# Kernel optimization log

Hardware: AMD Instinct MI355X
Metric: run time of the kernel (lower is better)

Reference implementation:

```python
import jax, jax.numpy as jnp
import numpy as np
import math

K = 8       # wavelet order (k)
C = 8       # channels (c)
ALPHA = 64  # retained Fourier modes
L = 0       # coarsest level
B = 32
N = 8192    # power of two


def setup_inputs() -> dict:
    key = jax.random.key(0)
    ks = jax.random.split(key, 14)
    ck = C * K
    scale = 1.0 / (ck * ck)  # matches torch: 1/(c*k)**2
    f32 = jnp.float32
    inp = {
        "x": jax.random.normal(ks[0], (B, N, C, K), dtype=f32),
        # SparseKernelFT1d weights (complex, stored as re/im): scale * rand
        "wA_re": scale * jax.random.uniform(ks[1], (ck, ck, ALPHA), dtype=f32),
        "wA_im": scale * jax.random.uniform(ks[2], (ck, ck, ALPHA), dtype=f32),
        "wB_re": scale * jax.random.uniform(ks[3], (ck, ck, ALPHA), dtype=f32),
        "wB_im": scale * jax.random.uniform(ks[4], (ck, ck, ALPHA), dtype=f32),
        "wC_re": scale * jax.random.uniform(ks[5], (ck, ck, ALPHA), dtype=f32),
        "wC_im": scale * jax.random.uniform(ks[6], (ck, ck, ALPHA), dtype=f32),
        # T0 linear layer (k -> k)
        "T0_w": jax.random.normal(ks[7], (K, K), dtype=f32) / math.sqrt(K),
        "T0_b": 0.01 * jax.random.normal(ks[8], (K,), dtype=f32),
        # Legendre wavelet filter buffers: ec_* are [H0.T;H1.T] / [G0.T;G1.T] (2k,k),
        # rc_* are [H0;G0] / [H1;G1] (2k,k). Stand-ins: random orthonormal-ish matrices
        # scaled like wavelet filters (same math regardless of exact values).
        "ec_s": jax.random.normal(ks[9], (2 * K, K), dtype=f32) / math.sqrt(2 * K),
        "ec_d": jax.random.normal(ks[10], (2 * K, K), dtype=f32) / math.sqrt(2 * K),
        "rc_e": jax.random.normal(ks[11], (2 * K, K), dtype=f32) / math.sqrt(2 * K),
        "rc_o": jax.random.normal(ks[12], (2 * K, K), dtype=f32) / math.sqrt(2 * K),
    }
    return inp


def _sparse_ft(x, w_re, w_im):
    # x: [B, N, c, k] -> spectral mixing over first ALPHA rfft modes
    Bb, Nn, c, k = x.shape
    xv = x.reshape(Bb, Nn, c * k).transpose(0, 2, 1)   # [B, ck, N]
    xf = jnp.fft.rfft(xv)                               # [B, ck, N//2+1] complex
    l = min(ALPHA, Nn // 2 + 1)
    W = (w_re[:, :, :l] + 1j * w_im[:, :, :l]).astype(jnp.complex64)
    of = jnp.einsum('bix,iox->box', xf[:, :, :l], W)
    out_ft = jnp.zeros((Bb, c * k, Nn // 2 + 1), dtype=jnp.complex64).at[:, :, :l].set(of)
    xo = jnp.fft.irfft(out_ft, n=Nn)                    # [B, ck, N] real
    return xo.transpose(0, 2, 1).reshape(Bb, Nn, c, k)


def reference(x, wA_re, wA_im, wB_re, wB_im, wC_re, wC_im, T0_w, T0_b,
              ec_s, ec_d, rc_e, rc_o):
    Bb, Nn, c, k = x.shape
    ns = int(math.floor(math.log2(Nn)))
    Ud, Us = [], []
    # --- decomposition ---
    for _ in range(ns - L):
        xa = jnp.concatenate([x[:, ::2], x[:, 1::2]], axis=-1)  # [B, N/2, c, 2k]
        d = xa @ ec_d                                           # [B, N/2, c, k]
        s = xa @ ec_s
        Ud.append(_sparse_ft(d, wA_re, wA_im) + _sparse_ft(s, wB_re, wB_im))
        Us.append(_sparse_ft(d, wC_re, wC_im))
        x = s
    # --- coarsest-level linear ---
    x = x @ T0_w.T + T0_b
    # --- reconstruction (u_s is None branch) ---
    for i in range(ns - 1 - L, -1, -1):
        x = x + Us[i]
        xc = jnp.concatenate([x, Ud[i]], axis=-1)               # [B, n, c, 2k]
        x_e = xc @ rc_e
        x_o = xc @ rc_o
        Bc, Nc, cc, _ = xc.shape
        x = jnp.stack([x_e, x_o], axis=2).reshape(Bc, Nc * 2, cc, K)  # interleave even/odd
    return (x,) + tuple(Ud) + tuple(Us)
```

## Files before the change

kernel.cpp:

```cpp
#include <hip/hip_runtime.h>

#define BB 32
#define CKD 64
#define CC 8
#define KK 8
#define TT 64
#define FPW 132

__device__ const int D_FCB[14] = {0,32,48,56,60,62,63,64,65,66,67,68,69,70};
__device__ const int D_TB[14] = {0,64,96,112,120,124,126,127,128,129,130,131,132,133};
__device__ const int D_LS[14] = {0,64,128,192,256,320,384,417,434,443,448,451,453,454};
__device__ const int D_L[13]  = {64,64,64,64,64,64,33,17,9,5,3,2,1};
__device__ const int D_FTOF[13] = {0,524288,786432,917504,983040,1015808,1032192,
                                   1048576,1064960,1081344,1097728,1114112,1130496};

typedef __attribute__((ext_vector_type(4))) short s4v;
typedef __attribute__((ext_vector_type(8))) short s8v;
typedef __attribute__((ext_vector_type(4))) float f4v;

static __device__ __forceinline__ float4 ld4(const float* p){ return *(const float4*)p; }
static __device__ __forceinline__ size_t d_udo(int i){ return 33554432ull - (16777216u >> i); }
static __device__ __forceinline__ size_t d_uso(int i){ return 50329600ull - (16777216u >> i); }
static __device__ __forceinline__ size_t d_tof(int i){ return 128ull * (8192u - (8192u >> i)); }

static __device__ __forceinline__ unsigned short b16(float f) {
    unsigned u = __float_as_uint(f);
    u += 0x7FFFu + ((u >> 16) & 1u);
    return (unsigned short)(u >> 16);
}
static __device__ __forceinline__ float fb16(unsigned short h) {
    return __uint_as_float(((unsigned)h) << 16);
}

__global__ __launch_bounds__(256) void gen_T_k(unsigned short* __restrict__ Th,
                                               unsigned short* __restrict__ Tl) {
    int lvl = blockIdx.y;
    int nh = 4096 >> lvl;
    int idx = blockIdx.x * 256 + threadIdx.x;
    if (idx >= nh * 128) return;
    int t = idx >> 7, k = idx & 127, x = k >> 1;
    int l = nh / 2 + 1; if (l > 64) l = 64;
    float v = 0.f;
    if (x < l) {
        int r = (x * t) & (nh - 1);
        float th = 6.283185307179586f * ((float)r / (float)nh);
        float s, c; sincosf(th, &s, &c);
        v = (k & 1) ? s : c;
    }
    unsigned short hi = b16(v);
    unsigned short lo = b16(v - fb16(hi));
    size_t off = d_tof(lvl) + idx;
    Th[off] = hi; Tl[off] = lo;
}

__global__ __launch_bounds__(256) void gen_Tf_k(unsigned short* __restrict__ Tfh,
                                                unsigned short* __restrict__ Tfl) {
    int lvl = blockIdx.y;
    int nh = 4096 >> lvl;
    int nhp = nh < 128 ? 128 : nh;
    int idx = blockIdx.x * 256 + threadIdx.x;
    if (idx >= 128 * nhp) return;
    int j = idx & 7;
    int lane = (idx >> 3) & 63;
    int mt = (idx >> 9) & 7;
    int kb = idx >> 12;
    int row = mt*16 + (lane & 15);
    int t = kb*32 + (lane >> 4)*8 + j;
    int x = row >> 1;
    int l = nh / 2 + 1; if (l > 64) l = 64;
    float v = 0.f;
    if (x < l && t < nh) {
        int r = (x * t) & (nh - 1);
        float th = 6.283185307179586f * ((float)r / (float)nh);
        float s, c; sincosf(th, &s, &c);
        v = (row & 1) ? -s : c;
    }
    unsigned short hi = b16(v);
    unsigned short lo = b16(v - fb16(hi));
    size_t off = (size_t)D_FTOF[lvl] + idx;
    Tfh[off] = hi; Tfl[off] = lo;
}

__global__ __launch_bounds__(256) void decomp_k(const float* __restrict__ xin,
        const float* __restrict__ ecd, const float* __restrict__ ecs,
        float* __restrict__ dslot, float* __restrict__ sslot, int nh) {
    int idx = blockIdx.x * 256 + threadIdx.x;
    if (idx >= BB * nh * CC) return;
    int c = idx & 7;
    int t = (idx >> 3) % nh;
    int b = idx / (nh * CC);
    const float* p0 = xin + ((size_t)b * 2 * nh + 2 * t) * CKD + c * KK;
    float xa[16];
    float4 v;
    v = ld4(p0);      xa[0]=v.x; xa[1]=v.y; xa[2]=v.z; xa[3]=v.w;
    v = ld4(p0+4);    xa[4]=v.x; xa[5]=v.y; xa[6]=v.z; xa[7]=v.w;
    v = ld4(p0+64);   xa[8]=v.x; xa[9]=v.y; xa[10]=v.z; xa[11]=v.w;
    v = ld4(p0+68);   xa[12]=v.x; xa[13]=v.y; xa[14]=v.z; xa[15]=v.w;
    float dd[8], ss[8];
    #pragma unroll
    for (int m = 0; m < 8; m++) { dd[m] = 0.f; ss[m] = 0.f; }
    #pragma unroll
    for (int j = 0; j < 16; j++) {
        float xv = xa[j];
        #pragma unroll
        for (int m = 0; m < 8; m++) {
            dd[m] = fmaf(xv, ecd[j*8+m], dd[m]);
            ss[m] = fmaf(xv, ecs[j*8+m], ss[m]);
        }
    }
    size_t ob = ((size_t)b * nh + t) * CKD + c * KK;
    *(float4*)(dslot+ob)   = make_float4(dd[0],dd[1],dd[2],dd[3]);
    *(float4*)(dslot+ob+4) = make_float4(dd[4],dd[5],dd[6],dd[7]);
    *(float4*)(sslot+ob)   = make_float4(ss[0],ss[1],ss[2],ss[3]);
    *(float4*)(sslot+ob+4) = make_float4(ss[4],ss[5],ss[6],ss[7]);
}

__global__ __launch_bounds__(256) void decomp_small_k(const float* __restrict__ s4base,
        const float* __restrict__ ecd, const float* __restrict__ ecs,
        const float* __restrict__ T0w, const float* __restrict__ T0b,
        float* __restrict__ outbuf, float* __restrict__ xt0) {
    __shared__ float sA[128*64];
    __shared__ float sB[64*64];
    int b = blockIdx.x, tid = threadIdx.x;
    for (int lvl = 5; lvl <= 12; lvl++) {
        int nh = 4096 >> lvl;
        const float* src = (lvl == 5) ? (s4base + (size_t)b*256*CKD)
                                      : (((lvl - 6) & 1) ? sB : sA);
        float* dst = ((lvl - 5) & 1) ? sB : sA;
        float* dG = outbuf + d_udo(lvl) + (size_t)b*nh*CKD;
        float* sG = outbuf + d_uso(lvl) + (size_t)b*nh*CKD;
        for (int q = tid; q < nh*8; q += 256) {
            int c = q & 7, t = q >> 3;
            const float* p0 = src + (size_t)(2*t)*CKD + c*KK;
            float xa[16];
            float4 v;
            v = ld4(p0);      xa[0]=v.x; xa[1]=v.y; xa[2]=v.z; xa[3]=v.w;
            v = ld4(p0+4);    xa[4]=v.x; xa[5]=v.y; xa[6]=v.z; xa[7]=v.w;
            v = ld4(p0+64);   xa[8]=v.x; xa[9]=v.y; xa[10]=v.z; xa[11]=v.w;
            v = ld4(p0+68);   xa[12]=v.x; xa[13]=v.y; xa[14]=v.z; xa[15]=v.w;
            float dd[8], ss[8];
            #pragma unroll
            for (int m = 0; m < 8; m++) { dd[m] = 0.f; ss[m] = 0.f; }
            #pragma unroll
            for (int j = 0; j < 16; j++) {
                float xv = xa[j];
                #pragma unroll
                for (int m = 0; m < 8; m++) {
                    dd[m] = fmaf(xv, ecd[j*8+m], dd[m]);
                    ss[m] = fmaf(xv, ecs[j*8+m], ss[m]);
                }
            }
            size_t ob = (size_t)t * CKD + c * KK;
            *(float4*)(dG+ob)   = make_float4(dd[0],dd[1],dd[2],dd[3]);
            *(float4*)(dG+ob+4) = make_float4(dd[4],dd[5],dd[6],dd[7]);
            *(float4*)(sG+ob)   = make_float4(ss[0],ss[1],ss[2],ss[3]);
            *(float4*)(sG+ob+4) = make_float4(ss[4],ss[5],ss[6],ss[7]);
            float* dl = dst + t*CKD + c*KK;
            #pragma unroll
            for (int j = 0; j < 8; j++) dl[j] = ss[j];
        }
        __syncthreads();
    }
    if (tid < 64) {
        int m = tid & 7, c = tid >> 3;
        const float* xr = sB + c*KK;
        float a = T0b[m];
        #pragma unroll
        for (int j = 0; j < 8; j++) a = fmaf(xr[j], T0w[m*8+j], a);
        xt0[(size_t)b*64 + tid] = a;
    }
}

__global__ __launch_bounds__(256) void fft_fwd_mfma_k(const float* __restrict__ outbuf,
        const unsigned short* __restrict__ Tfh, const unsigned short* __restrict__ Tfl,
        float* __restrict__ xfpf, float2* __restrict__ xf_all) {
    __shared__ unsigned vp[64*FPW];
    int slot = blockIdx.x;
    int lvl = 0;
    while (lvl < 12 && slot >= D_FCB[lvl+1]) lvl++;
    int nh = 4096 >> lvl;
    int ch = D_FCB[lvl+1] - D_FCB[lvl];
    int t0s = (slot - D_FCB[lvl]) * 128;
    int b = blockIdx.y, z = blockIdx.z;
    const float* V = outbuf + (z ? d_uso(lvl) : d_udo(lvl)) + (size_t)b * nh * CKD;
    const unsigned short* THb = Tfh + D_FTOF[lvl];
    const unsigned short* TLb = Tfl + D_FTOF[lvl];
    int tid = threadIdx.x;
    int w = tid >> 6, lane = tid & 63;
    int col = lane & 15, khi = lane >> 4;
    int mt0 = (w & 1) * 4, nt0 = (w >> 1) * 2;
    #pragma unroll
    for (int q = 0; q < 8; q++) {
        int fi = tid + 256*q;
        int tl_ = fi >> 4;
        int t = t0s + tl_;
        int i4 = (fi & 15) * 4;
        float4 v = make_float4(0.f,0.f,0.f,0.f);
        if (t < nh) v = ld4(V + (size_t)t*CKD + i4);
        const float* pv = &v.x;
        #pragma unroll
        for (int j = 0; j < 4; j++) {
            int row = i4 + j;
            float f = pv[j];
            unsigned u = __float_as_uint(f);
            unsigned hi = u & 0xFFFF0000u;
            float r = f - __uint_as_float(hi);
            unsigned lo = __float_as_uint(r) & 0xFFFF0000u;
            int cw = tl_ ^ (((row >> 3) & 7) << 2);
            vp[row*FPW + cw] = (hi >> 16) | lo;
        }
    }
    __syncthreads();
    int rrow[2], rswz[2];
    #pragma unroll
    for (int n = 0; n < 2; n++) {
        rrow[n] = (nt0 + n)*16 + col;
        rswz[n] = ((rrow[n] >> 3) & 7) << 2;
    }
    f4v acc[4][2];
    #pragma unroll
    for (int m = 0; m < 4; m++)
        #pragma unroll
        for (int n = 0; n < 2; n++) acc[m][n] = (f4v){0.f,0.f,0.f,0.f};
    int kb0 = (slot - D_FCB[lvl]) * 4;
    #pragma unroll
    for (int kk = 0; kk < 4; kk++) {
        int kb = kb0 + kk;
        s8v ah[4], al[4];
        #pragma unroll
        for (int m = 0; m < 4; m++) {
            size_t fo = (((size_t)kb*8 + (mt0 + m))*64 + lane)*8;
            ah[m] = *(const s8v*)(THb + fo);
            al[m] = *(const s8v*)(TLb + fo);
        }
        int cb = kk*32 + khi*8;
        #pragma unroll
        for (int n = 0; n < 2; n++) {
            const unsigned* pr = vp + rrow[n]*FPW;
            uint4 w0 = *(const uint4*)(pr + (cb ^ rswz[n]));
            uint4 w1 = *(const uint4*)(pr + ((cb + 4) ^ rswz[n]));
            s8v bh, bl;
            const unsigned* pw = &w0.x;
            #pragma unroll
            for (int j = 0; j < 4; j++) {
                bh[j] = (short)(pw[j] & 0xFFFFu);
                bl[j] = (short)(pw[j] >> 16);
            }
            pw = &w1.x;
            #pragma unroll
            for (int j = 0; j < 4; j++) {
                bh[4+j] = (short)(pw[j] & 0xFFFFu);
                bl[4+j] = (short)(pw[j] >> 16);
            }
            #pragma unroll
            for (int m = 0; m < 4; m++) {
                acc[m][n] = __builtin_amdgcn_mfma_f32_16x16x32_bf16(ah[m], bh, acc[m][n], 0,0,0);
                acc[m][n] = __builtin_amdgcn_mfma_f32_16x16x32_bf16(ah[m], bl, acc[m][n], 0,0,0);
                acc[m][n] = __builtin_amdgcn_mfma_f32_16x16x32_bf16(al[m], bh, acc[m][n], 0,0,0);
            }
        }
    }
    if (ch == 1) {
        float* X = (float*)xf_all + ((size_t)lvl*262144 + ((size_t)b*2 + z)*4096)*2;
        #pragma unroll
        for (int m = 0; m < 4; m++) {
            int m0 = (mt0 + m)*16 + khi*4;
            #pragma unroll
            for (int n = 0; n < 2; n++) {
                int ic = (nt0 + n)*16 + col;
                #pragma unroll
                for (int r = 0; r < 4; r++) {
                    int row = m0 + r;
                    X[(((size_t)(row >> 1)*64 + ic) << 1) | (row & 1)] = acc[m][n][r];
                }
            }
        }
    } else {
        float* P = xfpf + ((size_t)slot*64 + (size_t)b*2 + z) * 8192;
        #pragma unroll
        for (int m = 0; m < 4; m++) {
            int m0 = (mt0 + m)*16 + khi*4;
            #pragma unroll
            for (int n = 0; n < 2; n++) {
                int ic = (nt0 + n)*16 + col;
                #pragma unroll
                for (int r = 0; r < 4; r++)
                    P[(size_t)(m0 + r)*64 + ic] = acc[m][n][r];
            }
        }
    }
}

__global__ __launch_bounds__(256) void reduce_fwd_k(const float* __restrict__ xfpf,
        float2* __restrict__ xf_all) {
    int lvl = blockIdx.y;
    int e = blockIdx.x * 256 + threadIdx.x;
    int j = e & 4095;
    int bz = e >> 12;
    int x = j >> 6, i = j & 63;
    int c0 = D_FCB[lvl], c1 = D_FCB[lvl+1];
    float re = 0.f, im = 0.f;
    for (int c = c0; c < c1; c++) {
        size_t base = ((size_t)c*64 + bz) * 8192;
        re += xfpf[base + (size_t)(2*x)*64 + i];
        im += xfpf[base + (size_t)(2*x+1)*64 + i];
    }
    xf_all[(size_t)lvl*262144 + (size_t)bz*4096 + j] = make_float2(re, im);
}

__global__ __launch_bounds__(256) void mix_all_k(const float2* __restrict__ xf_all,
        const float* __restrict__ wAr, const float* __restrict__ wAi,
        const float* __restrict__ wBr, const float* __restrict__ wBi,
        const float* __restrict__ wCr, const float* __restrict__ wCi,
        unsigned short* __restrict__ ofh, unsigned short* __restrict__ ofl) {
    int lvl = 0;
    while (lvl < 12 && (int)blockIdx.x >= D_LS[lvl+1]) lvl++;
    int x = blockIdx.x - D_LS[lvl];
    int nh = 4096 >> lvl;
    const float2* xfL = xf_all + (size_t)lvl*262144;
    int tid = threadIdx.x;
    int o = tid & 63, wq = tid >> 6;
    __shared__ float2 sxd[BB*CKD];
    __shared__ float2 sxs[BB*CKD];
    __shared__ float  swt[6][16*CKD];
    for (int q = tid; q < BB*CKD; q += 256) {
        int b = q >> 6, i = q & 63;
        sxd[q] = xfL[((size_t)b*2 + 0)*4096 + x*64 + i];
        sxs[q] = xfL[((size_t)b*2 + 1)*4096 + x*64 + i];
    }
    float2 aud[8], aus[8];
    #pragma unroll
    for (int j=0;j<8;j++){ aud[j]=make_float2(0.f,0.f); aus[j]=make_float2(0.f,0.f); }
    for (int ic = 0; ic < 4; ic++) {
        __syncthreads();
        for (int q = tid; q < 16*CKD; q += 256) {
            int ii = q >> 6, oo = q & 63;
            size_t a = ((size_t)(ic*16+ii)*64 + oo)*64 + x;
            swt[0][q] = wAr[a]; swt[1][q] = wAi[a];
            swt[2][q] = wBr[a]; swt[3][q] = wBi[a];
            swt[4][q] = wCr[a]; swt[5][q] = wCi[a];
        }
        __syncthreads();
        #pragma unroll 4
        for (int ii = 0; ii < 16; ii++) {
            float ar = swt[0][ii*64+o], ai_ = swt[1][ii*64+o];
            float br = swt[2][ii*64+o], bi_ = swt[3][ii*64+o];
            float cr = swt[4][ii*64+o], ci_ = swt[5][ii*64+o];
            int i = ic*16 + ii;
            #pragma unroll
            for (int j = 0; j < 8; j++) {
                float2 xd = sxd[(wq*8+j)*64 + i];
                float2 xs = sxs[(wq*8+j)*64 + i];
                aud[j].x += xd.x*ar - xd.y*ai_ + xs.x*br - xs.y*bi_;
                aud[j].y += xd.x*ai_ + xd.y*ar + xs.x*bi_ + xs.y*br;
                aus[j].x += xd.x*cr - xd.y*ci_;
                aus[j].y += xd.x*ci_ + xd.y*cr;
            }
        }
    }
    float w = (x == 0 || 2*x == nh) ? 1.f : 2.f;
    float sc = w / (float)nh;
    int k0 = 2*x;
    #pragma unroll
    for (int j = 0; j < 8; j++) {
        int b = wq*8 + j;
        {
            size_t base = (((size_t)lvl*32 + b)*2 + 0)*8192;
            float A = sc*aud[j].x, Bn = -sc*aud[j].y;
            unsigned short ha = b16(A),  hb = b16(Bn);
            unsigned short la = b16(A - fb16(ha)), lb = b16(Bn - fb16(hb));
            ofh[base + (size_t)k0*64 + o]     = ha;
            ofh[base + (size_t)(k0+1)*64 + o] = hb;
            ofl[base + (size_t)k0*64 + o]     = la;
            ofl[base + (size_t)(k0+1)*64 + o] = lb;
        }
        {
            size_t base = (((size_t)lvl*32 + b)*2 + 1)*8192;
            float A = sc*aus[j].x, Bn = -sc*aus[j].y;
            unsigned short ha = b16(A),  hb = b16(Bn);
            unsigned short la = b16(A - fb16(ha)), lb = b16(Bn - fb16(hb));
            ofh[base + (size_t)k0*64 + o]     = ha;
            ofh[base + (size_t)(k0+1)*64 + o] = hb;
            ofl[base + (size_t)k0*64 + o]     = la;
            ofl[base + (size_t)(k0+1)*64 + o] = lb;
        }
    }
}

__global__ __launch_bounds__(256) void fft_inv_mfma_k(
        const unsigned short* __restrict__ ofh, const unsigned short* __restrict__ ofl,
        const unsigned short* __restrict__ Th,  const unsigned short* __restrict__ Tl,
        float* __restrict__ outbuf) {
    __shared__ unsigned short gh[64*132];
    __shared__ unsigned short gl[64*132];
    int lvl = 0;
    while (lvl < 12 && (int)blockIdx.x >= D_TB[lvl+1]) lvl++;
    int g = blockIdx.x - D_TB[lvl];
    int nh = 4096 >> lvl;
    int tbase = g * 64;
    int b = blockIdx.y, z = blockIdx.z;
    const unsigned short* Gh = ofh + (((size_t)lvl*32 + b)*2 + z)*8192;
    const unsigned short* Gl = ofl + (((size_t)lvl*32 + b)*2 + z)*8192;
    int tid = threadIdx.x;
    #pragma unroll
    for (int q = 0; q < 4; q++) {
        int fi = tid + 256*q;
        int k = fi & 127, oct = fi >> 7;
        uint4 vh = *(const uint4*)(Gh + (size_t)k*64 + oct*8);
        uint4 vl = *(const uint4*)(Gl + (size_t)k*64 + oct*8);
        const unsigned* ph = &vh.x;
        const unsigned* pl = &vl.x;
        #pragma unroll
        for (int i = 0; i < 8; i++) {
            unsigned wd = ph[i>>1];
            gh[(oct*8+i)*132 + k] = (i&1) ? (unsigned short)(wd>>16) : (unsigned short)(wd&0xFFFF);
            wd = pl[i>>1];
            gl[(oct*8+i)*132 + k] = (i&1) ? (unsigned short)(wd>>16) : (unsigned short)(wd&0xFFFF);
        }
    }
    __syncthreads();
    int w = tid >> 6;
    int lane = tid & 63;
    int tb = tbase + w*16;
    if (tb >= nh) return;
    int trow = lane & 15, khi = lane >> 4;
    int tA = tb + trow; if (tA >= nh) tA = nh - 1;
    const unsigned short* THp = Th + d_tof(lvl) + (size_t)tA*128 + khi*8;
    const unsigned short* TLp = Tl + d_tof(lvl) + (size_t)tA*128 + khi*8;
    f4v acc[4];
    #pragma unroll
    for (int n = 0; n < 4; n++) acc[n] = (f4v){0.f,0.f,0.f,0.f};
    #pragma unroll
    for (int kk = 0; kk < 4; kk++) {
        s8v ah = *(const s8v*)(THp + kk*32);
        s8v al = *(const s8v*)(TLp + kk*32);
        #pragma unroll
        for (int n = 0; n < 4; n++) {
            int off = (n*16 + trow)*132 + kk*32 + khi*8;
            s4v b0 = *(const s4v*)(gh + off);
            s4v b1 = *(const s4v*)(gh + off + 4);
            s4v c0 = *(const s4v*)(gl + off);
            s4v c1 = *(const s4v*)(gl + off + 4);
            s8v bh = __builtin_shufflevector(b0, b1, 0,1,2,3,4,5,6,7);
            s8v bl = __builtin_shufflevector(c0, c1, 0,1,2,3,4,5,6,7);
            acc[n] = __builtin_amdgcn_mfma_f32_16x16x32_bf16(ah, bh, acc[n], 0, 0, 0);
            acc[n] = __builtin_amdgcn_mfma_f32_16x16x32_bf16(ah, bl, acc[n], 0, 0, 0);
            acc[n] = __builtin_amdgcn_mfma_f32_16x16x32_bf16(al, bh, acc[n], 0, 0, 0);
        }
    }
    float* U = outbuf + (z ? d_uso(lvl) : d_udo(lvl)) + (size_t)b * nh * CKD;
    int thi4 = (lane >> 4) * 4;
    #pragma unroll
    for (int n = 0; n < 4; n++) {
        #pragma unroll
        for (int r = 0; r < 4; r++) {
            int t = tb + thi4 + r;
            if (t < nh) U[(size_t)t*64 + n*16 + trow] = acc[n][r];
        }
    }
}

__global__ __launch_bounds__(256) void recon_small_k(const float* __restrict__ xt0,
        const float* __restrict__ outbuf,
        const float* __restrict__ rce, const float* __restrict__ rco,
        float* __restrict__ rb0) {
    __shared__ float xA[128*64];
    __shared__ float xB[64*64];
    int b = blockIdx.x, tid = threadIdx.x;
    if (tid < 64) xB[tid] = xt0[(size_t)b*64 + tid];
    __syncthreads();
    for (int i = 12; i >= 6; i--) {
        int nh = 4096 >> i;
        const float* cur = ((i == 12) || !(i & 1)) ? xB : xA;
        float* nxt = (i & 1) ? xB : xA;
        const float* Us = outbuf + d_uso(i) + (size_t)b*nh*CKD;
        const float* Ud = outbuf + d_udo(i) + (size_t)b*nh*CKD;
        for (int q = tid; q < nh*8; q += 256) {
            int c = q & 7, t = q >> 3;
            size_t base = (size_t)t*CKD + c*KK;
            float xc[16];
            float4 a0 = ld4(cur+base), a1 = ld4(cur+base+4);
            float4 u0 = ld4(Us+base),  u1 = ld4(Us+base+4);
            float4 d0 = ld4(Ud+base),  d1 = ld4(Ud+base+4);
            xc[0]=a0.x+u0.x; xc[1]=a0.y+u0.y; xc[2]=a0.z+u0.z; xc[3]=a0.w+u0.w;
            xc[4]=a1.x+u1.x; xc[5]=a1.y+u1.y; xc[6]=a1.z+u1.z; xc[7]=a1.w+u1.w;
            xc[8]=d0.x;  xc[9]=d0.y;  xc[10]=d0.z; xc[11]=d0.w;
            xc[12]=d1.x; xc[13]=d1.y; xc[14]=d1.z; xc[15]=d1.w;
            float e[8], o2[8];
            #pragma unroll
            for (int m = 0; m < 8; m++) { e[m] = 0.f; o2[m] = 0.f; }
            #pragma unroll
            for (int j = 0; j < 16; j++) {
                float xv = xc[j];
                #pragma unroll
                for (int m = 0; m < 8; m++) {
                    e[m]  = fmaf(xv, rce[j*8+m], e[m]);
                    o2[m] = fmaf(xv, rco[j*8+m], o2[m]);
                }
            }
            if (i > 6) {
                float* pe = nxt + (size_t)(2*t)*CKD + c*KK;
                #pragma unroll
                for (int j = 0; j < 8; j++) { pe[j] = e[j]; pe[CKD + j] = o2[j]; }
            } else {
                float* pe = rb0 + ((size_t)b*128 + 2*t)*CKD + c*KK;
                *(float4*)(pe)      = make_float4(e[0],e[1],e[2],e[3]);
                *(float4*)(pe+4)    = make_float4(e[4],e[5],e[6],e[7]);
                *(float4*)(pe+64)   = make_float4(o2[0],o2[1],o2[2],o2[3]);
                *(float4*)(pe+68)   = make_float4(o2[4],o2[5],o2[6],o2[7]);
            }
        }
        __syncthreads();
    }
}

__global__ __launch_bounds__(256) void recon_k(const float* __restrict__ xin,
        const float* __restrict__ us, const float* __restrict__ ud,
        const float* __restrict__ rce, const float* __restrict__ rco,
        float* __restrict__ xout, int nh) {
    int idx = blockIdx.x*256 + threadIdx.x;
    if (idx >= BB*nh*CC) return;
    int c = idx & 7;
    int t = (idx >> 3) % nh;
    int b = idx / (nh*CC);
    size_t base = ((size_t)b*nh + t)*CKD + c*KK;
    float xc[16];
    float4 a0 = ld4(xin+base), a1 = ld4(xin+base+4);
    float4 u0 = ld4(us+base),  u1 = ld4(us+base+4);
    float4 d0 = ld4(ud+base),  d1 = ld4(ud+base+4);
    xc[0]=a0.x+u0.x; xc[1]=a0.y+u0.y; xc[2]=a0.z+u0.z; xc[3]=a0.w+u0.w;
    xc[4]=a1.x+u1.x; xc[5]=a1.y+u1.y; xc[6]=a1.z+u1.z; xc[7]=a1.w+u1.w;
    xc[8]=d0.x;  xc[9]=d0.y;  xc[10]=d0.z; xc[11]=d0.w;
    xc[12]=d1.x; xc[13]=d1.y; xc[14]=d1.z; xc[15]=d1.w;
    float e[8], o2[8];
    #pragma unroll
    for (int m = 0; m < 8; m++) { e[m] = 0.f; o2[m] = 0.f; }
    #pragma unroll
    for (int j = 0; j < 16; j++) {
        float xv = xc[j];
        #pragma unroll
        for (int m = 0; m < 8; m++) {
            e[m]  = fmaf(xv, rce[j*8+m], e[m]);
            o2[m] = fmaf(xv, rco[j*8+m], o2[m]);
        }
    }
    size_t ob = ((size_t)b*2*nh + 2*t)*CKD + c*KK;
    *(float4*)(xout+ob)      = make_float4(e[0],e[1],e[2],e[3]);
    *(float4*)(xout+ob+4)    = make_float4(e[4],e[5],e[6],e[7]);
    *(float4*)(xout+ob+64)   = make_float4(o2[0],o2[1],o2[2],o2[3]);
    *(float4*)(xout+ob+68)   = make_float4(o2[4],o2[5],o2[6],o2[7]);
}

extern "C" void kernel_launch(void* const* d_in, const int* in_sizes, int n_in,
                              void* d_out, int out_size, void* d_ws, size_t ws_size,
                              hipStream_t stream) {
    const float* x   = (const float*)d_in[0];
    const float* wAr = (const float*)d_in[1];
    const float* wAi = (const float*)d_in[2];
    const float* wBr = (const float*)d_in[3];
    const float* wBi = (const float*)d_in[4];
    const float* wCr = (const float*)d_in[5];
    const float* wCi = (const float*)d_in[6];
    const float* T0w = (const float*)d_in[7];
    const float* T0b = (const float*)d_in[8];
    const float* ecs = (const float*)d_in[9];
    const float* ecd = (const float*)d_in[10];
    const float* rce = (const float*)d_in[11];
    const float* rco = (const float*)d_in[12];
    float* out = (float*)d_out;
    float* wsf = (float*)d_ws;

    size_t p = 0;
    float2* xf_all = (float2*)(wsf + p); p += 6815744;
    unsigned short* ofh = (unsigned short*)(wsf + p); p += 3407872;
    unsigned short* ofl = (unsigned short*)(wsf + p); p += 3407872;
    unsigned short* Th  = (unsigned short*)(wsf + p); p += 528384;
    unsigned short* Tl  = (unsigned short*)(wsf + p); p += 528384;
    unsigned short* Tfh = (unsigned short*)(wsf + p); p += 573440;
    unsigned short* Tfl = (unsigned short*)(wsf + p); p += 573440;
    float*  xt0  = wsf + p; p += 2048;
    float*  rb0  = wsf + p; p += 4194304;
    float*  rb1  = wsf + p; p += 8388608;
    float*  xfpf = wsf + p; p += 36700160;
    (void)ws_size; (void)in_sizes; (void)n_in; (void)out_size;

    size_t udo[13], uso[13];
    for (int i = 0; i < 13; i++) {
        udo[i] = 33554432ull - (16777216u >> i);
        uso[i] = 50329600ull - (16777216u >> i);
    }

    gen_T_k<<<dim3(2048, 13), 256, 0, stream>>>(Th, Tl);
    gen_Tf_k<<<dim3(2048, 13), 256, 0, stream>>>(Tfh, Tfl);

    for (int i = 0; i < 5; i++) {
        int nh = 4096 >> i;
        const float* xin_l = (i == 0) ? x : (out + uso[i-1]);
        int tot = BB * nh * CC;
        decomp_k<<<(tot + 255)/256, 256, 0, stream>>>(xin_l, ecd, ecs, out + udo[i], out + uso[i], nh);
    }
    decomp_small_k<<<BB, 256, 0, stream>>>(out + uso[4], ecd, ecs, T0w, T0b, out, xt0);

    fft_fwd_mfma_k<<<dim3(70, BB, 2), 256, 0, stream>>>(out, Tfh, Tfl, xfpf, xf_all);
    reduce_fwd_k<<<dim3(1024, 5), 256, 0, stream>>>(xfpf, xf_all);
    mix_all_k<<<454, 256, 0, stream>>>(xf_all, wAr, wAi, wBr, wBi, wCr, wCi, ofh, ofl);
    fft_inv_mfma_k<<<dim3(133, BB, 2), 256, 0, stream>>>(ofh, ofl, Th, Tl, out);

    recon_small_k<<<BB, 256, 0, stream>>>(xt0, out, rce, rco, rb0);
    const float* rin = rb0;
    for (int i = 5; i >= 0; i--) {
        int nh = 4096 >> i;
        float* ro = (i == 0) ? out : ((i & 1) ? rb1 : rb0);
        int tot = BB * nh * CC;
        recon_k<<<(tot + 255)/256, 256, 0, stream>>>(rin, out + uso[i], out + udo[i], rce, rco, ro, nh);
        rin = ro;
    }
}
```

Before: 489.7 us.

## Merge d/s halves in forward and inverse MFMA DFT kernels to reuse twiddles

Result: no change. 481.0 us (-1.8%).

```diff
diff --git a/kernel.cpp b/kernel.cpp
--- a/kernel.cpp
+++ b/kernel.cpp
@@ -4,7 +4,6 @@
 #define CKD 64
 #define CC 8
 #define KK 8
-#define TT 64
 #define FPW 132
 
 __device__ const int D_FCB[14] = {0,32,48,56,60,62,63,64,65,66,67,68,69,70};
@@ -32,53 +31,50 @@
     return __uint_as_float(((unsigned)h) << 16);
 }
 
-__global__ __launch_bounds__(256) void gen_T_k(unsigned short* __restrict__ Th,
-                                               unsigned short* __restrict__ Tl) {
+__global__ __launch_bounds__(256) void gen_tbl2_k(unsigned short* __restrict__ Th,
+        unsigned short* __restrict__ Tl, unsigned short* __restrict__ Tfh,
+        unsigned short* __restrict__ Tfl) {
     int lvl = blockIdx.y;
     int nh = 4096 >> lvl;
     int idx = blockIdx.x * 256 + threadIdx.x;
-    if (idx >= nh * 128) return;
-    int t = idx >> 7, k = idx & 127, x = k >> 1;
-    int l = nh / 2 + 1; if (l > 64) l = 64;
-    float v = 0.f;
-    if (x < l) {
-        int r = (x * t) & (nh - 1);
-        float th = 6.283185307179586f * ((float)r / (float)nh);
-        float s, c; sincosf(th, &s, &c);
-        v = (k & 1) ? s : c;
-    }
-    unsigned short hi = b16(v);
-    unsigned short lo = b16(v - fb16(hi));
-    size_t off = d_tof(lvl) + idx;
-    Th[off] = hi; Tl[off] = lo;
-}
-
-__global__ __launch_bounds__(256) void gen_Tf_k(unsigned short* __restrict__ Tfh,
-                                                unsigned short* __restrict__ Tfl) {
-    int lvl = blockIdx.y;
-    int nh = 4096 >> lvl;
-    int nhp = nh < 128 ? 128 : nh;
-    int idx = blockIdx.x * 256 + threadIdx.x;
-    if (idx >= 128 * nhp) return;
-    int j = idx & 7;
-    int lane = (idx >> 3) & 63;
-    int mt = (idx >> 9) & 7;
-    int kb = idx >> 12;
-    int row = mt*16 + (lane & 15);
-    int t = kb*32 + (lane >> 4)*8 + j;
-    int x = row >> 1;
-    int l = nh / 2 + 1; if (l > 64) l = 64;
-    float v = 0.f;
-    if (x < l && t < nh) {
-        int r = (x * t) & (nh - 1);
-        float th = 6.283185307179586f * ((float)r / (float)nh);
-        float s, c; sincosf(th, &s, &c);
-        v = (row & 1) ? -s : c;
-    }
-    unsigned short hi = b16(v);
-    unsigned short lo = b16(v - fb16(hi));
-    size_t off = (size_t)D_FTOF[lvl] + idx;
-    Tfh[off] = hi; Tfl[off] = lo;
+    if (blockIdx.z == 0) {
+        if (idx >= nh * 128) return;
+        int t = idx >> 7, k = idx & 127, x = k >> 1;
+        int l = nh / 2 + 1; if (l > 64) l = 64;
+        float v = 0.f;
+        if (x < l) {
+            int r = (x * t) & (nh - 1);
+            float th = 6.283185307179586f * ((float)r / (float)nh);
+            float s, c; sincosf(th, &s, &c);
+            v = (k & 1) ? s : c;
+        }
+        unsigned short hi = b16(v);
+        unsigned short lo = b16(v - fb16(hi));
+        size_t off = d_tof(lvl) + idx;
+        Th[off] = hi; Tl[off] = lo;
+    } else {
+        int nhp = nh < 128 ? 128 : nh;
+        if (idx >= 128 * nhp) return;
+        int j = idx & 7;
+        int lane = (idx >> 3) & 63;
+        int mt = (idx >> 9) & 7;
+        int kb = idx >> 12;
+        int row = mt*16 + (lane & 15);
+        int t = kb*32 + (lane >> 4)*8 + j;
+        int x = row >> 1;
+        int l = nh / 2 + 1; if (l > 64) l = 64;
+        float v = 0.f;
+        if (x < l && t < nh) {
+            int r = (x * t) & (nh - 1);
+            float th = 6.283185307179586f * ((float)r / (float)nh);
+            float s, c; sincosf(th, &s, &c);
+            v = (row & 1) ? -s : c;
+        }
+        unsigned short hi = b16(v);
+        unsigned short lo = b16(v - fb16(hi));
+        size_t off = (size_t)D_FTOF[lvl] + idx;
+        Tfh[off] = hi; Tfl[off] = lo;
+    }
 }
 
 __global__ __launch_bounds__(256) void decomp_k(const float* __restrict__ xin,
@@ -174,33 +170,38 @@
 __global__ __launch_bounds__(256) void fft_fwd_mfma_k(const float* __restrict__ outbuf,
         const unsigned short* __restrict__ Tfh, const unsigned short* __restrict__ Tfl,
         float* __restrict__ xfpf, float2* __restrict__ xf_all) {
-    __shared__ unsigned vp[64*FPW];
+    __shared__ unsigned vp[128*FPW];
     int slot = blockIdx.x;
     int lvl = 0;
     while (lvl < 12 && slot >= D_FCB[lvl+1]) lvl++;
     int nh = 4096 >> lvl;
     int ch = D_FCB[lvl+1] - D_FCB[lvl];
     int t0s = (slot - D_FCB[lvl]) * 128;
-    int b = blockIdx.y, z = blockIdx.z;
-    const float* V = outbuf + (z ? d_uso(lvl) : d_udo(lvl)) + (size_t)b * nh * CKD;
+    int b = blockIdx.y;
+    const float* V0 = outbuf + d_udo(lvl) + (size_t)b * nh * CKD;
+    const float* V1 = outbuf + d_uso(lvl) + (size_t)b * nh * CKD;
     const unsigned short* THb = Tfh + D_FTOF[lvl];
     const unsigned short* TLb = Tfl + D_FTOF[lvl];
     int tid = threadIdx.x;
     int w = tid >> 6, lane = tid & 63;
     int col = lane & 15, khi = lane >> 4;
-    int mt0 = (w & 1) * 4, nt0 = (w >> 1) * 2;
-    #pragma unroll
-    for (int q = 0; q < 8; q++) {
+    int mt0 = w * 2;
+    #pragma unroll
+    for (int q = 0; q < 16; q++) {
         int fi = tid + 256*q;
-        int tl_ = fi >> 4;
+        int tl_ = fi >> 5;
         int t = t0s + tl_;
-        int i4 = (fi & 15) * 4;
+        int iq = fi & 31;
+        int z = iq >> 4;
+        int i4 = (iq & 15) * 4;
+        const float* Vz = z ? V1 : V0;
         float4 v = make_float4(0.f,0.f,0.f,0.f);
-        if (t < nh) v = ld4(V + (size_t)t*CKD + i4);
+        if (t < nh) v = ld4(Vz + (size_t)t*CKD + i4);
         const float* pv = &v.x;
+        int rowb = z*64 + i4;
         #pragma unroll
         for (int j = 0; j < 4; j++) {
-            int row = i4 + j;
+            int row = rowb + j;
             float f = pv[j];
             unsigned u = __float_as_uint(f);
             unsigned hi = u & 0xFFFF0000u;
@@ -211,31 +212,31 @@
         }
     }
     __syncthreads();
-    int rrow[2], rswz[2];
-    #pragma unroll
-    for (int n = 0; n < 2; n++) {
-        rrow[n] = (nt0 + n)*16 + col;
+    int rrow[8], rswz[8];
+    #pragma unroll
+    for (int n = 0; n < 8; n++) {
+        rrow[n] = n*16 + col;
         rswz[n] = ((rrow[n] >> 3) & 7) << 2;
     }
-    f4v acc[4][2];
-    #pragma unroll
-    for (int m = 0; m < 4; m++)
-        #pragma unroll
-        for (int n = 0; n < 2; n++) acc[m][n] = (f4v){0.f,0.f,0.f,0.f};
+    f4v acc[2][8];
+    #pragma unroll
+    for (int m = 0; m < 2; m++)
+        #pragma unroll
+        for (int n = 0; n < 8; n++) acc[m][n] = (f4v){0.f,0.f,0.f,0.f};
     int kb0 = (slot - D_FCB[lvl]) * 4;
     #pragma unroll
     for (int kk = 0; kk < 4; kk++) {
         int kb = kb0 + kk;
-        s8v ah[4], al[4];
-        #pragma unroll
-        for (int m = 0; m < 4; m++) {
+        s8v ah[2], al[2];
+        #pragma unroll
+        for (int m = 0; m < 2; m++) {
             size_t fo = (((size_t)kb*8 + (mt0 + m))*64 + lane)*8;
             ah[m] = *(const s8v*)(THb + fo);
             al[m] = *(const s8v*)(TLb + fo);
         }
         int cb = kk*32 + khi*8;
         #pragma unroll
-        for (int n = 0; n < 2; n++) {
+        for (int n = 0; n < 8; n++) {
             const unsigned* pr = vp + rrow[n]*FPW;
             uint4 w0 = *(const uint4*)(pr + (cb ^ rswz[n]));
             uint4 w1 = *(const uint4*)(pr + ((cb + 4) ^ rswz[n]));
@@ -253,7 +254,7 @@
                 bl[4+j] = (short)(pw[j] >> 16);
             }
             #pragma unroll
-            for (int m = 0; m < 4; m++) {
+            for (int m = 0; m < 2; m++) {
                 acc[m][n] = __builtin_amdgcn_mfma_f32_16x16x32_bf16(ah[m], bh, acc[m][n], 0,0,0);
                 acc[m][n] = __builtin_amdgcn_mfma_f32_16x16x32_bf16(ah[m], bl, acc[m][n], 0,0,0);
                 acc[m][n] = __builtin_amdgcn_mfma_f32_16x16x32_bf16(al[m], bh, acc[m][n], 0,0,0);
@@ -261,31 +262,34 @@
         }
     }
     if (ch == 1) {
-        float* X = (float*)xf_all + ((size_t)lvl*262144 + ((size_t)b*2 + z)*4096)*2;
-        #pragma unroll
-        for (int m = 0; m < 4; m++) {
+        float* XB = (float*)xf_all + (size_t)lvl*524288 + (size_t)b*16384;
+        #pragma unroll
+        for (int m = 0; m < 2; m++) {
             int m0 = (mt0 + m)*16 + khi*4;
             #pragma unroll
-            for (int n = 0; n < 2; n++) {
-                int ic = (nt0 + n)*16 + col;
+            for (int n = 0; n < 8; n++) {
+                int ic = n*16 + col;
+                int z = ic >> 6, i = ic & 63;
+                float* X = XB + (size_t)z*8192;
                 #pragma unroll
                 for (int r = 0; r < 4; r++) {
                     int row = m0 + r;
-                    X[(((size_t)(row >> 1)*64 + ic) << 1) | (row & 1)] = acc[m][n][r];
+                    X[(((size_t)(row >> 1)*64 + i) << 1) | (row & 1)] = acc[m][n][r];
                 }
             }
         }
     } else {
-        float* P = xfpf + ((size_t)slot*64 + (size_t)b*2 + z) * 8192;
-        #pragma unroll
-        for (int m = 0; m < 4; m++) {
+        #pragma unroll
+        for (int m = 0; m < 2; m++) {
             int m0 = (mt0 + m)*16 + khi*4;
             #pragma unroll
-            for (int n = 0; n < 2; n++) {
-                int ic = (nt0 + n)*16 + col;
+            for (int n = 0; n < 8; n++) {
+                int ic = n*16 + col;
+                int z = ic >> 6, i = ic & 63;
+                float* P = xfpf + ((size_t)slot*64 + (size_t)b*2 + z) * 8192;
                 #pragma unroll
                 for (int r = 0; r < 4; r++)
-                    P[(size_t)(m0 + r)*64 + ic] = acc[m][n][r];
+                    P[(size_t)(m0 + r)*64 + i] = acc[m][n][r];
             }
         }
     }
@@ -391,21 +395,23 @@
         const unsigned short* __restrict__ ofh, const unsigned short* __restrict__ ofl,
         const unsigned short* __restrict__ Th,  const unsigned short* __restrict__ Tl,
         float* __restrict__ outbuf) {
-    __shared__ unsigned short gh[64*132];
-    __shared__ unsigned short gl[64*132];
+    __shared__ unsigned short gh[2*64*132];
+    __shared__ unsigned short gl[2*64*132];
     int lvl = 0;
     while (lvl < 12 && (int)blockIdx.x >= D_TB[lvl+1]) lvl++;
     int g = blockIdx.x - D_TB[lvl];
     int nh = 4096 >> lvl;
     int tbase = g * 64;
-    int b = blockIdx.y, z = blockIdx.z;
-    const unsigned short* Gh = ofh + (((size_t)lvl*32 + b)*2 + z)*8192;
-    const unsigned short* Gl = ofl + (((size_t)lvl*32 + b)*2 + z)*8192;
+    int b = blockIdx.y;
     int tid = threadIdx.x;
     #pragma unroll
-    for (int q = 0; q < 4; q++) {
+    for (int q = 0; q < 8; q++) {
         int fi = tid + 256*q;
-        int k = fi & 127, oct = fi >> 7;
+        int z = fi >> 10;
+        int r = fi & 1023;
+        int k = r & 127, oct = r >> 7;
+        const unsigned short* Gh = ofh + (((size_t)lvl*32 + b)*2 + z)*8192;
+        const unsigned short* Gl = ofl + (((size_t)lvl*32 + b)*2 + z)*8192;
         uint4 vh = *(const uint4*)(Gh + (size_t)k*64 + oct*8);
         uint4 vl = *(const uint4*)(Gl + (size_t)k*64 + oct*8);
         const unsigned* ph = &vh.x;
@@ -413,9 +419,9 @@
         #pragma unroll
         for (int i = 0; i < 8; i++) {
             unsigned wd = ph[i>>1];
-            gh[(oct*8+i)*132 + k] = (i&1) ? (unsigned short)(wd>>16) : (unsigned short)(wd&0xFFFF);
+            gh[z*8448 + (oct*8+i)*132 + k] = (i&1) ? (unsigned short)(wd>>16) : (unsigned short)(wd&0xFFFF);
             wd = pl[i>>1];
-            gl[(oct*8+i)*132 + k] = (i&1) ? (unsigned short)(wd>>16) : (unsigned short)(wd&0xFFFF);
+            gl[z*8448 + (oct*8+i)*132 + k] = (i&1) ? (unsigned short)(wd>>16) : (unsigned short)(wd&0xFFFF);
         }
     }
     __syncthreads();
@@ -427,16 +433,17 @@
     int tA = tb + trow; if (tA >= nh) tA = nh - 1;
     const unsigned short* THp = Th + d_tof(lvl) + (size_t)tA*128 + khi*8;
     const unsigned short* TLp = Tl + d_tof(lvl) + (size_t)tA*128 + khi*8;
-    f4v acc[4];
-    #pragma unroll
-    for (int n = 0; n < 4; n++) acc[n] = (f4v){0.f,0.f,0.f,0.f};
+    f4v acc[8];
+    #pragma unroll
+    for (int n = 0; n < 8; n++) acc[n] = (f4v){0.f,0.f,0.f,0.f};
     #pragma unroll
     for (int kk = 0; kk < 4; kk++) {
         s8v ah = *(const s8v*)(THp + kk*32);
         s8v al = *(const s8v*)(TLp + kk*32);
         #pragma unroll
-        for (int n = 0; n < 4; n++) {
-            int off = (n*16 + trow)*132 + kk*32 + khi*8;
+        for (int n = 0; n < 8; n++) {
+            int z = n >> 2;
+            int off = z*8448 + ((n & 3)*16 + trow)*132 + kk*32 + khi*8;
             s4v b0 = *(const s4v*)(gh + off);
             s4v b1 = *(const s4v*)(gh + off + 4);
             s4v c0 = *(const s4v*)(gl + off);
@@ -448,14 +455,17 @@
             acc[n] = __builtin_amdgcn_mfma_f32_16x16x32_bf16(al, bh, acc[n], 0, 0, 0);
         }
     }
-    float* U = outbuf + (z ? d_uso(lvl) : d_udo(lvl)) + (size_t)b * nh * CKD;
-    int thi4 = (lane >> 4) * 4;
-    #pragma unroll
-    for (int n = 0; n < 4; n++) {
+    float* U0 = outbuf + d_udo(lvl) + (size_t)b * nh * CKD;
+    float* U1 = outbuf + d_uso(lvl) + (size_t)b * nh * CKD;
+    int thi4 = khi * 4;
+    #pragma unroll
+    for (int n = 0; n < 8; n++) {
+        float* U = (n >> 2) ? U1 : U0;
+        int ocol = (n & 3)*16 + trow;
         #pragma unroll
         for (int r = 0; r < 4; r++) {
             int t = tb + thi4 + r;
-            if (t < nh) U[(size_t)t*64 + n*16 + trow] = acc[n][r];
+            if (t < nh) U[(size_t)t*64 + ocol] = acc[n][r];
         }
     }
 }
@@ -590,8 +600,7 @@
         uso[i] = 50329600ull - (16777216u >> i);
     }
 
-    gen_T_k<<<dim3(2048, 13), 256, 0, stream>>>(Th, Tl);
-    gen_Tf_k<<<dim3(2048, 13), 256, 0, stream>>>(Tfh, Tfl);
+    gen_tbl2_k<<<dim3(2048, 13, 2), 256, 0, stream>>>(Th, Tl, Tfh, Tfl);
 
     for (int i = 0; i < 5; i++) {
         int nh = 4096 >> i;
@@ -601,10 +610,10 @@
     }
     decomp_small_k<<<BB, 256, 0, stream>>>(out + uso[4], ecd, ecs, T0w, T0b, out, xt0);
 
-    fft_fwd_mfma_k<<<dim3(70, BB, 2), 256, 0, stream>>>(out, Tfh, Tfl, xfpf, xf_all);
+    fft_fwd_mfma_k<<<dim3(70, BB), 256, 0, stream>>>(out, Tfh, Tfl, xfpf, xf_all);
     reduce_fwd_k<<<dim3(1024, 5), 256, 0, stream>>>(xfpf, xf_all);
     mix_all_k<<<454, 256, 0, stream>>>(xf_all, wAr, wAi, wBr, wBi, wCr, wCi, ofh, ofl);
-    fft_inv_mfma_k<<<dim3(133, BB, 2), 256, 0, stream>>>(ofh, ofl, Th, Tl, out);
+    fft_inv_mfma_k<<<dim3(133, BB), 256, 0, stream>>>(ofh, ofl, Th, Tl, out);
 
     recon_small_k<<<BB, 256, 0, stream>>>(xt0, out, rce, rco, rb0);
     const float* rin = rb0;
```
